# Optimization experiments

Hardware: AMD Instinct MI355X
Metric: run time of the kernel (lower is better)

Reference implementation:

```python
import jax, jax.numpy as jnp
import numpy as np

B, N, E = 4, 4096, 16384
D, A_DIM = 256, 64
T, HALF, STEPS, NTYPES = 16, 8, 3, 50


def setup_inputs() -> dict:
    key = jax.random.key(0)
    ks = jax.random.split(key, 16)
    s = 0.02  # small init so repeated DxD matmuls stay stable over 3 steps
    return {
        "annotation_id": jax.random.randint(ks[0], (B, N), 0, NTYPES),
        "src": jax.random.randint(ks[1], (B, E), 0, N),
        "dst": jax.random.randint(ks[2], (B, E), 0, N),
        "etype": jax.random.randint(ks[3], (B, E), 0, HALF),
        "edge_embed": jax.random.normal(ks[4], (T, D * D), jnp.float32) * s,
        "edge_bias": jax.random.normal(ks[5], (T, D), jnp.float32) * s,
        "type_embed": jax.random.normal(ks[6], (NTYPES, A_DIM), jnp.float32) * s,
        "Wr": jax.random.normal(ks[7], (D, 3 * D), jnp.float32) * s,
        "br": jnp.zeros((D,), jnp.float32),
        "Wz": jax.random.normal(ks[8], (D, 3 * D), jnp.float32) * s,
        "bz": jnp.zeros((D,), jnp.float32),
        "Wh": jax.random.normal(ks[9], (D, 3 * D), jnp.float32) * s,
        "bh": jnp.zeros((D,), jnp.float32),
        "Wa": jax.random.normal(ks[10], (1, D + A_DIM), jnp.float32) * s,
        "ba": jnp.zeros((1,), jnp.float32),
        "Wo": jax.random.normal(ks[11], (1, D + A_DIM), jnp.float32) * s,
        "bo": jnp.zeros((1,), jnp.float32),
    }


def reference(annotation_id, src, dst, etype, edge_embed, edge_bias, type_embed,
              Wr, br, Wz, bz, Wh, bh, Wa, ba, Wo, bo):
    # annotation: typeEmbed[id-1] if id>0 else zeros  -> [B, N, A_DIM]
    ann = jnp.where((annotation_id > 0)[..., None],
                    type_embed[jnp.clip(annotation_id - 1, 0, NTYPES - 1)],
                    jnp.zeros((), type_embed.dtype))
    # prop_state: annotation zero-padded to state_dim  -> [B, N, D]
    h = jnp.concatenate([ann, jnp.zeros((B, N, D - A_DIM), ann.dtype)], axis=-1)
    W = edge_embed.reshape(T, D, D)  # per-edge-type DxD matrices

    def step(h):
        # type-major projection: apply every edge-type matrix to every node state
        # P[b, t, n, :] = W[t] @ h[b, n]   -> [B, T, N, D]
        P = jnp.einsum('tij,bnj->btni', W, h)

        def per_graph(Pg, s_, d_, e_):
            # a_out[j]        += W[e] @ h[neighbour] + b[e]
            # a_in[neighbour] += W[e+HALF] @ h[j]   + b[e+HALF]
            m_out = Pg[e_, d_] + edge_bias[e_]            # [E, D]
            m_in = Pg[e_ + HALF, s_] + edge_bias[e_ + HALF]
            a_out = jnp.zeros((N, D), h.dtype).at[s_].add(m_out)
            a_in = jnp.zeros((N, D), h.dtype).at[d_].add(m_in)
            return a_in, a_out

        a_in, a_out = jax.vmap(per_graph)(P, src, dst, etype)
        # GRU-style propagator (dropout_rate = 0 -> identity)
        a = jnp.concatenate([a_in, a_out, h], axis=-1)    # [B, N, 3D]
        r = jax.nn.sigmoid(a @ Wr.T + br)
        z = jax.nn.sigmoid(a @ Wz.T + bz)
        h_hat = jnp.tanh(jnp.concatenate([a_in, a_out, r * h], axis=-1) @ Wh.T + bh)
        return (1.0 - z) * h + z * h_hat

    for _ in range(STEPS):
        h = step(h)

    join = jnp.concatenate([h, ann], axis=-1)             # [B, N, D+A]
    atten = jax.nn.sigmoid(join @ Wa.T + ba)              # [B, N, 1]
    ou = jnp.tanh(join @ Wo.T + bo)                       # [B, N, 1]
    w_sum = jnp.sum((atten * ou).reshape(-1, N), axis=1)  # [B]
    return jax.nn.sigmoid(w_sum)
```

## Files before the change

kernel.cpp:

```cpp
#include <hip/hip_runtime.h>
#include <cstdint>

#define BB 4
#define NN 4096
#define EE 16384
#define DD 256
#define ADIM 64
#define TT 16
#define HALFE 8
#define STEPS 3
#define OSTRIDE 4160
#define MAXTILES 1088
#define MAXM (MAXTILES * 128)

#define AS1 __attribute__((address_space(1)))
#define AS3 __attribute__((address_space(3)))

typedef __attribute__((ext_vector_type(8))) short short8;
typedef __attribute__((ext_vector_type(4))) float f32x4;

__device__ __forceinline__ float sigmoidf_(float x) { return 1.0f / (1.0f + __expf(-x)); }

__device__ __forceinline__ unsigned short f2bf(float x) {
    unsigned u = __float_as_uint(x);
    u += 0x7fffu + ((u >> 16) & 1u);
    return (unsigned short)(u >> 16);
}
__device__ __forceinline__ float bf2f(unsigned short b) {
    return __uint_as_float(((unsigned)b) << 16);
}

__global__ void prep_kernel(const int* __restrict__ ann_id, const float* __restrict__ type_embed,
                            const float* __restrict__ edge_embed, const float* __restrict__ Wr,
                            const float* __restrict__ Wz, const float* __restrict__ Wh,
                            float* __restrict__ ann, float* __restrict__ h,
                            unsigned short* __restrict__ hbf, unsigned short* __restrict__ Xbf,
                            unsigned short* __restrict__ W2bf, unsigned short* __restrict__ Wcatbf,
                            unsigned short* __restrict__ Whhbf, float* __restrict__ acc) {
    int bid = blockIdx.x, tid = threadIdx.x;
    if (bid < 4096) {
        if (bid == 0 && tid < 16) acc[tid] = 0.f;
        int idx = bid * 256 + tid;
        int bn = idx >> 6, q = idx & 63;
        int id = ann_id[bn];
        float4 v = {0.f, 0.f, 0.f, 0.f};
        if (q < 16) {
            if (id > 0) v = ((const float4*)(type_embed + (size_t)(id - 1) * ADIM))[q];
            ((float4*)(ann + (size_t)bn * ADIM))[q] = v;
        }
        ((float4*)(h + (size_t)bn * DD))[q] = v;
        ushort4 o;
        o.x = f2bf(v.x); o.y = f2bf(v.y); o.z = f2bf(v.z); o.w = f2bf(v.w);
        ((ushort4*)(hbf + (size_t)bn * DD))[q] = o;
        ((ushort4*)(Xbf + (size_t)bn * 768 + 512))[q] = o;
    } else if (bid < 5120) {
        int idx = (bid - 4096) * 256 + tid;
        float4 v = ((const float4*)edge_embed)[idx];
        ushort4 o;
        o.x = f2bf(v.x); o.y = f2bf(v.y); o.z = f2bf(v.z); o.w = f2bf(v.w);
        ((ushort4*)W2bf)[idx] = o;
    } else if (bid < 7424) {
        int idx = (bid - 5120) * 256 + tid;
        int c = idx / 768, k = idx % 768;
        float v;
        if (c < 256)       v = Wr[c * 768 + k];
        else if (c < 512)  v = Wz[(c - 256) * 768 + k];
        else               v = (k < 512) ? Wh[(c - 512) * 768 + k] : 0.f;
        Wcatbf[idx] = f2bf(v);
    } else {
        int idx = (bid - 7424) * 256 + tid;
        int i = idx / 256, k = idx % 256;
        Whhbf[idx] = f2bf(Wh[i * 768 + 512 + k]);
    }
}

__global__ void count_all(const int* __restrict__ src, const int* __restrict__ dst,
                          const int* __restrict__ et, int* __restrict__ counts,
                          int* __restrict__ c32) {
    __shared__ int cnt[32];
    int tid = threadIdx.x;
    if (tid < 32) cnt[tid] = 0;
    __syncthreads();
    int idx = blockIdx.x * 256 + tid;
    int b = idx >> 14;
    atomicAdd(&counts[(b * 2 + 0) * NN + src[idx]], 1);
    atomicAdd(&counts[(b * 2 + 1) * NN + dst[idx]], 1);
    atomicAdd(&cnt[b * 8 + et[idx]], 1);
    __syncthreads();
    if (tid < 32) atomicAdd(&c32[tid], cnt[tid]);
}

__global__ __launch_bounds__(1024) void scan_kernel(const int* __restrict__ counts,
                                                    int* __restrict__ offs,
                                                    int* __restrict__ cursor) {
    __shared__ int lsum[1024];
    int t = threadIdx.x, seg = blockIdx.x;
    int4 v = ((const int4*)(counts + (size_t)seg * NN))[t];
    int s1 = v.x + v.y, s2 = s1 + v.z, s3 = s2 + v.w;
    lsum[t] = s3;
    __syncthreads();
    for (int off = 1; off < 1024; off <<= 1) {
        int tmp = (t >= off) ? lsum[t - off] : 0;
        __syncthreads();
        lsum[t] += tmp;
        __syncthreads();
    }
    int base = lsum[t] - s3;
    int* o = offs + (size_t)seg * OSTRIDE;
    o[4 * t] = base; o[4 * t + 1] = base + v.x; o[4 * t + 2] = base + s1; o[4 * t + 3] = base + s2;
    if (t == 1023) o[4096] = lsum[1023];
    int* c = cursor + (size_t)seg * NN;
    c[4 * t] = base; c[4 * t + 1] = base + v.x; c[4 * t + 2] = base + s1; c[4 * t + 3] = base + s2;
}

__global__ void scan2_kernel(const int* __restrict__ c32, int* __restrict__ type_cursor,
                             int* __restrict__ tile_type, int* __restrict__ idx2) {
    __shared__ int pad[64];
    int t = threadIdx.x;
    for (int k = t; k < MAXTILES; k += 64) tile_type[k] = -1;
    __syncthreads();
    int b = t >> 4, dir = (t >> 3) & 1, tt = t & 7;
    int cnt = c32[b * 8 + tt];
    int padded = ((cnt + 127) >> 7) << 7;
    pad[t] = padded;
    __syncthreads();
    int off = 0;
    for (int k = 0; k < t; ++k) off += pad[k];
    type_cursor[t] = off;
    int t16 = dir * 8 + tt;
    int tile0 = off >> 7;
    for (int k = 0; k < (padded >> 7); ++k) tile_type[tile0 + k] = t16;
    for (int r = off + cnt; r < off + padded; ++r) idx2[r] = 0;
}

__global__ void fill2_kernel(const int* __restrict__ src, const int* __restrict__ dst,
                             const int* __restrict__ et, int* __restrict__ type_cursor,
                             int* __restrict__ node_cursor, int* __restrict__ entries,
                             int* __restrict__ idx2) {
    __shared__ int cnt[64];
    __shared__ int bse[64];
    int tid = threadIdx.x;
    if (tid < 64) cnt[tid] = 0;
    __syncthreads();
    int idx = blockIdx.x * 256 + tid;
    int b = idx >> 14;
    int s = src[idx], d = dst[idx], t = et[idx];
    int bin0 = b * 16 + t;
    int bin1 = b * 16 + 8 + t;
    int r0 = atomicAdd(&cnt[bin0], 1);
    int r1 = atomicAdd(&cnt[bin1], 1);
    __syncthreads();
    if (tid < 64) bse[tid] = atomicAdd(&type_cursor[tid], cnt[tid]);
    __syncthreads();
    int p0 = bse[bin0] + r0;
    int p1 = bse[bin1] + r1;
    idx2[p0] = b * NN + d;
    idx2[p1] = b * NN + s;
    int q0 = atomicAdd(&node_cursor[(b * 2 + 0) * NN + s], 1);
    entries[(size_t)(b * 2 + 0) * EE + q0] = (p0 << 4) | t;
    int q1 = atomicAdd(&node_cursor[(b * 2 + 1) * NN + d], 1);
    entries[(size_t)(b * 2 + 1) * EE + q1] = (p1 << 4) | (t + 8);
}


#define COMP_128x64(cb)                                                                 \
    _Pragma("unroll")                                                                   \
    for (int kk = 0; kk < 2; ++kk) {                                                    \
        short8 af[4], bfv[2];                                                           \
        _Pragma("unroll")                                                               \
        for (int m = 0; m < 4; ++m) {                                                   \
            int R = wr * 64 + m * 16 + lr;                                              \
            af[m] = *(const short8*)((const char*)As + (cb) * 16384 + R * 128 + (((kk * 4 + hi) ^ rx) << 4)); \
        }                                                                               \
        _Pragma("unroll")                                                               \
        for (int n = 0; n < 2; ++n) {                                                   \
            int R = wc * 32 + n * 16 + lr;                                              \
            bfv[n] = *(const short8*)((const char*)Bs + (cb) * 8192 + R * 128 + (((kk * 4 + hi) ^ rx) << 4)); \
        }                                                                               \
        _Pragma("unroll")                                                               \
        for (int m = 0; m < 4; ++m)                                                     \
            _Pragma("unroll")                                                           \
            for (int n = 0; n < 2; ++n)                                                 \
                acc[m][n] = __builtin_amdgcn_mfma_f32_16x16x32_bf16(bfv[n], af[m], acc[m][n], 0, 0, 0); \
    }

#define PIPE_WAIT(NSTR)                                                                 \
    asm volatile("s_waitcnt vmcnt(" NSTR ")" ::: "memory");                             \
    __builtin_amdgcn_s_barrier();                                                       \
    __builtin_amdgcn_sched_barrier(0);

__global__ __launch_bounds__(256) void gemm_msgs(const unsigned short* __restrict__ A,
                                                 const unsigned short* __restrict__ W2,
                                                 const int* __restrict__ idx2,
                                                 const int* __restrict__ tile_type,
                                                 unsigned short* __restrict__ C) {
    __shared__ __align__(16) unsigned short As[2 * 128 * 64];
    __shared__ __align__(16) unsigned short Bs[2 * 64 * 64];
    const int bid = blockIdx.x;
    const int wg = (bid & 7) * (MAXTILES * 4 / 8) + (bid >> 3);
    const int by = wg >> 2, bx = wg & 3;
    const int t16 = tile_type[by];
    if (t16 < 0) return;
    const int r0 = by << 7, c0 = bx << 6;
    const int tid = threadIdx.x;
    const int wv = tid >> 6, lane = tid & 63;
    const int wr = wv >> 1, wc = wv & 1;
    const int lr = lane & 15, hi = lane >> 4, rx = lane & 7;
    const int srow = wv * 8 + (lane >> 3);
    const int scol = ((lane & 7) ^ (lane >> 3)) << 3;
    int ar[4];
#pragma unroll
    for (int i = 0; i < 4; ++i) ar[i] = idx2[r0 + srow + i * 32];
    const unsigned short* Bg = W2 + (size_t)t16 * (DD * DD) + (size_t)(c0 + srow) * DD + scol;
    f32x4 acc[4][2] = {};
#define MS_STG(buf, kof)                                                                \
    { _Pragma("unroll")                                                                 \
      for (int i = 0; i < 4; ++i)                                                       \
          __builtin_amdgcn_global_load_lds(                                             \
              (const AS1 void*)(A + (size_t)ar[i] * DD + scol + (kof)),                 \
              (AS3 void*)((char*)As + (buf) * 16384 + wv * 1024 + i * 4096), 16, 0, 0); \
      _Pragma("unroll")                                                                 \
      for (int i = 0; i < 2; ++i)                                                       \
          __builtin_amdgcn_global_load_lds(                                             \
              (const AS1 void*)(Bg + (size_t)(i * 32) * DD + (kof)),                    \
              (AS3 void*)((char*)Bs + (buf) * 8192 + wv * 1024 + i * 4096), 16, 0, 0); }
    MS_STG(0, 0)
    for (int it = 0; it < 3; ++it) {
        MS_STG((it + 1) & 1, (it + 1) * 64)
        PIPE_WAIT("6")
        COMP_128x64(it & 1)
        __builtin_amdgcn_s_barrier();
    }
    PIPE_WAIT("0")
    COMP_128x64(1)
    const int erow = r0 + wr * 64 + lr;
    const int ecol = c0 + wc * 32 + (hi << 2);
#pragma unroll
    for (int m = 0; m < 4; ++m)
#pragma unroll
        for (int n = 0; n < 2; ++n) {
            ushort4 o;
            o.x = f2bf(acc[m][n][0]); o.y = f2bf(acc[m][n][1]);
            o.z = f2bf(acc[m][n][2]); o.w = f2bf(acc[m][n][3]);
            *(ushort4*)&C[(size_t)(erow + m * 16) * DD + ecol + n * 16] = o;
        }
}

__global__ __launch_bounds__(256) void gemm_rzu(const unsigned short* __restrict__ A,
                                                const unsigned short* __restrict__ Bt,
                                                const float* __restrict__ br,
                                                const float* __restrict__ bz,
                                                const float* __restrict__ h,
                                                unsigned short* __restrict__ RH,
                                                unsigned short* __restrict__ Zb,
                                                unsigned short* __restrict__ Ub) {
    __shared__ __align__(16) unsigned short As[2 * 128 * 64];
    __shared__ __align__(16) unsigned short Bs[2 * 64 * 64];
    const int bid = blockIdx.x;
    const int wg = (bid & 7) * 192 + (bid >> 3);
    const int bx = wg % 12, by = wg / 12;
    const int r0 = by << 7, c0 = bx << 6;
    const int tid = threadIdx.x;
    const int wv = tid >> 6, lane = tid & 63;
    const int wr = wv >> 1, wc = wv & 1;
    const int lr = lane & 15, hi = lane >> 4, rx = lane & 7;
    const int srow = wv * 8 + (lane >> 3);
    const int scol = ((lane & 7) ^ (lane >> 3)) << 3;
    const unsigned short* Ag = A + (size_t)(r0 + srow) * 768 + scol;
    const unsigned short* Bg = Bt + (size_t)(c0 + srow) * 768 + scol;
    f32x4 acc[4][2] = {};
#define RZ_STG(buf, kof)                                                                \
    { _Pragma("unroll")                                                                 \
      for (int i = 0; i < 4; ++i)                                                       \
          __builtin_amdgcn_global_load_lds(                                             \
              (const AS1 void*)(Ag + (size_t)(i * 32) * 768 + (kof)),                   \
              (AS3 void*)((char*)As + (buf) * 16384 + wv * 1024 + i * 4096), 16, 0, 0); \
      _Pragma("unroll")                                                                 \
      for (int i = 0; i < 2; ++i)                                                       \
          __builtin_amdgcn_global_load_lds(                                             \
              (const AS1 void*)(Bg + (size_t)(i * 32) * 768 + (kof)),                   \
              (AS3 void*)((char*)Bs + (buf) * 8192 + wv * 1024 + i * 4096), 16, 0, 0); }
    RZ_STG(0, 0)
    for (int it = 0; it < 11; ++it) {
        RZ_STG((it + 1) & 1, (it + 1) * 64)
        PIPE_WAIT("6")
        COMP_128x64(it & 1)
        __builtin_amdgcn_s_barrier();
    }
    PIPE_WAIT("0")
    COMP_128x64(1)
    const int erow = r0 + wr * 64 + lr;
    const int ecol = c0 + wc * 32 + (hi << 2);
    const int region = c0 >> 8;
#pragma unroll
    for (int m = 0; m < 4; ++m)
#pragma unroll
        for (int n = 0; n < 2; ++n) {
            int gr = erow + m * 16;
            int gc = ecol + n * 16;
            f32x4 v = acc[m][n];
            if (region == 0) {
                float4 bb = *(const float4*)&br[gc];
                float4 hv = *(const float4*)&h[(size_t)gr * 256 + gc];
                ushort4 o;
                o.x = f2bf(sigmoidf_(v[0] + bb.x) * hv.x);
                o.y = f2bf(sigmoidf_(v[1] + bb.y) * hv.y);
                o.z = f2bf(sigmoidf_(v[2] + bb.z) * hv.z);
                o.w = f2bf(sigmoidf_(v[3] + bb.w) * hv.w);
                *(ushort4*)&RH[(size_t)gr * 256 + gc] = o;
            } else if (region == 1) {
                int c = gc - 256;
                float4 bb = *(const float4*)&bz[c];
                ushort4 o;
                o.x = f2bf(sigmoidf_(v[0] + bb.x));
                o.y = f2bf(sigmoidf_(v[1] + bb.y));
                o.z = f2bf(sigmoidf_(v[2] + bb.z));
                o.w = f2bf(sigmoidf_(v[3] + bb.w));
                *(ushort4*)&Zb[(size_t)gr * 256 + c] = o;
            } else {
                int c = gc - 512;
                ushort4 o;
                o.x = f2bf(v[0]); o.y = f2bf(v[1]); o.z = f2bf(v[2]); o.w = f2bf(v[3]);
                *(ushort4*)&Ub[(size_t)gr * 256 + c] = o;
            }
        }
}

__global__ __launch_bounds__(256) void gemm_hh(const unsigned short* __restrict__ A,
                                               const unsigned short* __restrict__ Bt,
                                               const unsigned short* __restrict__ Zb,
                                               const unsigned short* __restrict__ Ub,
                                               const float* __restrict__ bh,
                                               float* __restrict__ h,
                                               unsigned short* __restrict__ hbf,
                                               unsigned short* __restrict__ Xbf) {
    __shared__ __align__(16) unsigned short As[2 * 64 * 64];
    __shared__ __align__(16) unsigned short Bs[2 * 64 * 64];
    const int bid = blockIdx.x;
    const int wg = (bid & 7) * 128 + (bid >> 3);
    const int by = wg >> 2, bx = wg & 3;
    const int r0 = by << 6, c0 = bx << 6;
    const int tid = threadIdx.x;
    const int wv = tid >> 6, lane = tid & 63;
    const int wr = wv >> 1, wc = wv & 1;
    const int lr = lane & 15, hi = lane >> 4, rx = lane & 7;
    const int srow = wv * 8 + (lane >> 3);
    const int scol = ((lane & 7) ^ (lane >> 3)) << 3;
    const unsigned short* Ag = A + (size_t)(r0 + srow) * 256 + scol;
    const unsigned short* Bg = Bt + (size_t)(c0 + srow) * 256 + scol;
    f32x4 acc[2][2] = {};
#define HH_STG(buf, kof)                                                                \
    { _Pragma("unroll")                                                                 \
      for (int i = 0; i < 2; ++i) {                                                     \
          __builtin_amdgcn_global_load_lds(                                             \
              (const AS1 void*)(Ag + (size_t)(i * 32) * 256 + (kof)),                   \
              (AS3 void*)((char*)As + (buf) * 8192 + wv * 1024 + i * 4096), 16, 0, 0);  \
          __builtin_amdgcn_global_load_lds(                                             \
              (const AS1 void*)(Bg + (size_t)(i * 32) * 256 + (kof)),                   \
              (AS3 void*)((char*)Bs + (buf) * 8192 + wv * 1024 + i * 4096), 16, 0, 0); } }
#define COMP_64x64(cb)                                                                  \
    _Pragma("unroll")                                                                   \
    for (int kk = 0; kk < 2; ++kk) {                                                    \
        short8 af[2], bfv[2];                                                           \
        _Pragma("unroll")                                                               \
        for (int m = 0; m < 2; ++m) {                                                   \
            int R = wr * 32 + m * 16 + lr;                                              \
            af[m] = *(const short8*)((const char*)As + (cb) * 8192 + R * 128 + (((kk * 4 + hi) ^ rx) << 4)); \
        }                                                                               \
        _Pragma("unroll")                                                               \
        for (int n = 0; n < 2; ++n) {                                                   \
            int R = wc * 32 + n * 16 + lr;                                              \
            bfv[n] = *(const short8*)((const char*)Bs + (cb) * 8192 + R * 128 + (((kk * 4 + hi) ^ rx) << 4)); \
        }                                                                               \
        _Pragma("unroll")                                                               \
        for (int m = 0; m < 2; ++m)                                                     \
            _Pragma("unroll")                                                           \
            for (int n = 0; n < 2; ++n)                                                 \
                acc[m][n] = __builtin_amdgcn_mfma_f32_16x16x32_bf16(bfv[n], af[m], acc[m][n], 0, 0, 0); \
    }
    HH_STG(0, 0)
    for (int it = 0; it < 3; ++it) {
        HH_STG((it + 1) & 1, (it + 1) * 64)
        PIPE_WAIT("4")
        COMP_64x64(it & 1)
        __builtin_amdgcn_s_barrier();
    }
    PIPE_WAIT("0")
    COMP_64x64(1)
    const int erow = r0 + wr * 32 + lr;
    const int ecol = c0 + wc * 32 + (hi << 2);
#pragma unroll
    for (int m = 0; m < 2; ++m)
#pragma unroll
        for (int n = 0; n < 2; ++n) {
            int gr = erow + m * 16;
            int gc = ecol + n * 16;
            size_t base = (size_t)gr * 256 + gc;
            f32x4 v = acc[m][n];
            float4 bb = *(const float4*)&bh[gc];
            float4 hv = *(const float4*)&h[base];
            ushort4 zp = *(const ushort4*)&Zb[base];
            ushort4 up = *(const ushort4*)&Ub[base];
            float4 hn;
            {
                float z = bf2f(zp.x); hn.x = (1.f - z) * hv.x + z * tanhf(bf2f(up.x) + v[0] + bb.x);
            }{
                float z = bf2f(zp.y); hn.y = (1.f - z) * hv.y + z * tanhf(bf2f(up.y) + v[1] + bb.y);
            }{
                float z = bf2f(zp.z); hn.z = (1.f - z) * hv.z + z * tanhf(bf2f(up.z) + v[2] + bb.z);
            }{
                float z = bf2f(zp.w); hn.w = (1.f - z) * hv.w + z * tanhf(bf2f(up.w) + v[3] + bb.w);
            }
            *(float4*)&h[base] = hn;
            ushort4 o;
            o.x = f2bf(hn.x); o.y = f2bf(hn.y); o.z = f2bf(hn.z); o.w = f2bf(hn.w);
            *(ushort4*)&hbf[base] = o;
            *(ushort4*)&Xbf[(size_t)gr * 768 + 512 + gc] = o;
        }
}

__global__ void gather2_kernel(const unsigned short* __restrict__ msgs,
                               const int* __restrict__ offs, const int* __restrict__ entries,
                               const float* __restrict__ bias, unsigned short* __restrict__ Xb) {
    int wv = threadIdx.x >> 6, lane = threadIdx.x & 63;
    int slot = blockIdx.x * 4 + wv;
    int b = slot >> 13;
    int dir = (slot >> 12) & 1;
    int node = slot & 4095;
    const int* o = offs + (size_t)(b * 2 + dir) * OSTRIDE;
    int beg = o[node], end = o[node + 1];
    const int* ent = entries + (size_t)(b * 2 + dir) * EE;
    const float4* bias4 = (const float4*)bias;
    float4 acc = {0.f, 0.f, 0.f, 0.f};
    for (int p = beg; p < end; ++p) {
        int e2 = ent[p];
        int row = e2 >> 4, t = e2 & 15;
        ushort4 pv = *(const ushort4*)(msgs + (size_t)row * DD + lane * 4);
        float4 bv = bias4[t * 64 + lane];
        acc.x += bf2f(pv.x) + bv.x;
        acc.y += bf2f(pv.y) + bv.y;
        acc.z += bf2f(pv.z) + bv.z;
        acc.w += bf2f(pv.w) + bv.w;
    }
    ushort4 o4;
    o4.x = f2bf(acc.x); o4.y = f2bf(acc.y); o4.z = f2bf(acc.z); o4.w = f2bf(acc.w);
    int colbase = (dir == 0 ? 256 : 0) + lane * 4;
    *(ushort4*)(Xb + ((size_t)b * NN + node) * 768 + colbase) = o4;
}

__global__ void final_reduce(const float* __restrict__ h, const float* __restrict__ ann,
                             const float* __restrict__ Wa, const float* __restrict__ ba,
                             const float* __restrict__ Wo, const float* __restrict__ bo,
                             float* __restrict__ acc) {
    int wv = threadIdx.x >> 6, lane = threadIdx.x & 63;
    int b = blockIdx.x >> 5;
    int nbase = (blockIdx.x & 31) * 128 + wv * 32;
    float4 wah = ((const float4*)Wa)[lane];
    float4 woh = ((const float4*)Wo)[lane];
    float4 waa = {0, 0, 0, 0}, woa = {0, 0, 0, 0};
    if (lane < 16) {
        waa = ((const float4*)(Wa + 256))[lane];
        woa = ((const float4*)(Wo + 256))[lane];
    }
    float bav = ba[0], bov = bo[0];
    float part = 0.f;
    for (int it = 0; it < 32; ++it) {
        int node = nbase + it;
        float4 hv = ((const float4*)(h + ((size_t)b * NN + node) * DD))[lane];
        float sa = hv.x * wah.x + hv.y * wah.y + hv.z * wah.z + hv.w * wah.w;
        float so = hv.x * woh.x + hv.y * woh.y + hv.z * woh.z + hv.w * woh.w;
        if (lane < 16) {
            float4 av = ((const float4*)(ann + ((size_t)b * NN + node) * ADIM))[lane];
            sa += av.x * waa.x + av.y * waa.y + av.z * waa.z + av.w * waa.w;
            so += av.x * woa.x + av.y * woa.y + av.z * woa.z + av.w * woa.w;
        }
        for (int off = 32; off; off >>= 1) {
            sa += __shfl_down(sa, off);
            so += __shfl_down(so, off);
        }
        if (lane == 0) part += sigmoidf_(sa + bav) * tanhf(so + bov);
    }
    if (lane == 0) atomicAdd(&acc[b], part);
}

__global__ void final_out(const float* __restrict__ acc, float* __restrict__ out) {
    int b = threadIdx.x;
    if (b < BB) out[b] = sigmoidf_(acc[b]);
}

extern "C" void kernel_launch(void* const* d_in, const int* in_sizes, int n_in,
                              void* d_out, int out_size, void* d_ws, size_t ws_size,
                              hipStream_t stream) {
    const int*   ann_id     = (const int*)d_in[0];
    const int*   src        = (const int*)d_in[1];
    const int*   dst        = (const int*)d_in[2];
    const int*   etype      = (const int*)d_in[3];
    const float* edge_embed = (const float*)d_in[4];
    const float* edge_bias  = (const float*)d_in[5];
    const float* type_embed = (const float*)d_in[6];
    const float* Wr = (const float*)d_in[7];
    const float* br = (const float*)d_in[8];
    const float* Wz = (const float*)d_in[9];
    const float* bz = (const float*)d_in[10];
    const float* Wh = (const float*)d_in[11];
    const float* bh = (const float*)d_in[12];
    const float* Wa = (const float*)d_in[13];
    const float* ba = (const float*)d_in[14];
    const float* Wo = (const float*)d_in[15];
    const float* bo = (const float*)d_in[16];
    float* out = (float*)d_out;

    char* base = (char*)d_ws;
    size_t off = 0;
    auto alloc = [&](size_t bytes) { char* p = base + off; off += (bytes + 255) & ~(size_t)255; return p; };
    float* ann  = (float*)alloc((size_t)BB * NN * ADIM * 4);
    float* h    = (float*)alloc((size_t)BB * NN * DD * 4);
    float* acc  = (float*)alloc(64);
    unsigned short* h_bf   = (unsigned short*)alloc((size_t)BB * NN * DD * 2);
    unsigned short* W2bf   = (unsigned short*)alloc((size_t)TT * DD * DD * 2);
    unsigned short* Wcatbf = (unsigned short*)alloc(768 * 768 * 2);
    unsigned short* Whhbf  = (unsigned short*)alloc(256 * 256 * 2);
    unsigned short* msgs   = (unsigned short*)alloc((size_t)MAXM * DD * 2);
    unsigned short* Xbf    = (unsigned short*)alloc((size_t)BB * NN * 768 * 2);
    unsigned short* RHbf   = (unsigned short*)alloc((size_t)BB * NN * DD * 2);
    unsigned short* Zb     = (unsigned short*)alloc((size_t)BB * NN * DD * 2);
    unsigned short* Ub     = (unsigned short*)alloc((size_t)BB * NN * DD * 2);
    int* counts  = (int*)alloc((size_t)BB * 2 * NN * 4);
    int* c32     = (int*)alloc(32 * 4);
    int* cursor  = (int*)alloc((size_t)BB * 2 * NN * 4);
    int* offsets = (int*)alloc((size_t)BB * 2 * OSTRIDE * 4);
    int* entries = (int*)alloc((size_t)BB * 2 * EE * 4);
    int* tcur    = (int*)alloc(64 * 4);
    int* ttype   = (int*)alloc(MAXTILES * 4);
    int* idx2    = (int*)alloc((size_t)MAXM * 4);

    prep_kernel<<<dim3(7680), dim3(256), 0, stream>>>(
        ann_id, type_embed, edge_embed, Wr, Wz, Wh,
        ann, h, h_bf, Xbf, W2bf, Wcatbf, Whhbf, acc);
    hipMemsetAsync(counts, 0, (size_t)BB * 2 * NN * 4 + 256, stream);
    count_all<<<dim3((BB * EE) / 256), dim3(256), 0, stream>>>(src, dst, etype, counts, c32);
    scan_kernel<<<dim3(BB * 2), dim3(1024), 0, stream>>>(counts, offsets, cursor);
    scan2_kernel<<<dim3(1), dim3(64), 0, stream>>>(c32, tcur, ttype, idx2);
    fill2_kernel<<<dim3((BB * EE) / 256), dim3(256), 0, stream>>>(
        src, dst, etype, tcur, cursor, entries, idx2);

    for (int s = 0; s < STEPS; ++s) {
        gemm_msgs<<<dim3(MAXTILES * 4), dim3(256), 0, stream>>>(
            h_bf, W2bf, idx2, ttype, msgs);
        gather2_kernel<<<dim3(BB * 2 * NN / 4), dim3(256), 0, stream>>>(
            msgs, offsets, entries, edge_bias, Xbf);
        gemm_rzu<<<dim3(1536), dim3(256), 0, stream>>>(
            Xbf, Wcatbf, br, bz, h, RHbf, Zb, Ub);
        gemm_hh<<<dim3(1024), dim3(256), 0, stream>>>(
            RHbf, Whhbf, Zb, Ub, bh, h, h_bf, Xbf);
    }

    final_reduce<<<dim3(128), dim3(256), 0, stream>>>(h, ann, Wa, ba, Wo, bo, acc);
    final_out<<<dim3(1), dim3(64), 0, stream>>>(acc, out);
}
```

Baseline: 410.8 us.

## Enlarge message and gate GEMM tiles to 256x64 with 512-thread blocks

The gathered-message GEMM and the r/z/u gate GEMM move from 128x64 tiles with 4 waves to 256x64 tiles with 8 waves. Per-type padding goes from 128 to 256 rows and the tile count and launch grids shrink to match. Each W tile loaded into LDS is now reused across twice as many rows, which cuts B-operand traffic and the number of blocks. The cost is more LDS per block, more padding waste per edge type, and fewer blocks to spread across CUs. The counts memset is also folded into the prep kernel to drop one launch.

```diff
diff --git a/kernel.cpp b/kernel.cpp
--- a/kernel.cpp
+++ b/kernel.cpp
@@ -10,8 +10,8 @@
 #define HALFE 8
 #define STEPS 3
 #define OSTRIDE 4160
-#define MAXTILES 1088
-#define MAXM (MAXTILES * 128)
+#define MT2 640
+#define MAXM (MT2 * 256)
 
 #define AS1 __attribute__((address_space(1)))
 #define AS3 __attribute__((address_space(3)))
@@ -36,9 +36,12 @@
                             float* __restrict__ ann, float* __restrict__ h,
                             unsigned short* __restrict__ hbf, unsigned short* __restrict__ Xbf,
                             unsigned short* __restrict__ W2bf, unsigned short* __restrict__ Wcatbf,
-                            unsigned short* __restrict__ Whhbf, float* __restrict__ acc) {
+                            unsigned short* __restrict__ Whhbf, float* __restrict__ acc,
+                            int* __restrict__ counts, int* __restrict__ c32) {
     int bid = blockIdx.x, tid = threadIdx.x;
     if (bid < 4096) {
+        if (bid < 128) counts[bid * 256 + tid] = 0;
+        if (bid == 0 && tid < 32) c32[tid] = 0;
         if (bid == 0 && tid < 16) acc[tid] = 0.f;
         int idx = bid * 256 + tid;
         int bn = idx >> 6, q = idx & 63;
@@ -117,19 +120,19 @@
                              int* __restrict__ tile_type, int* __restrict__ idx2) {
     __shared__ int pad[64];
     int t = threadIdx.x;
-    for (int k = t; k < MAXTILES; k += 64) tile_type[k] = -1;
+    for (int k = t; k < MT2; k += 64) tile_type[k] = -1;
     __syncthreads();
     int b = t >> 4, dir = (t >> 3) & 1, tt = t & 7;
     int cnt = c32[b * 8 + tt];
-    int padded = ((cnt + 127) >> 7) << 7;
+    int padded = ((cnt + 255) >> 8) << 8;
     pad[t] = padded;
     __syncthreads();
     int off = 0;
     for (int k = 0; k < t; ++k) off += pad[k];
     type_cursor[t] = off;
     int t16 = dir * 8 + tt;
-    int tile0 = off >> 7;
-    for (int k = 0; k < (padded >> 7); ++k) tile_type[tile0 + k] = t16;
+    int tile0 = off >> 8;
+    for (int k = 0; k < (padded >> 8); ++k) tile_type[tile0 + k] = t16;
     for (int r = off + cnt; r < off + padded; ++r) idx2[r] = 0;
 }
 
@@ -163,18 +166,23 @@
 }
 
 
-#define COMP_128x64(cb)                                                                 \
+#define PIPE_WAIT(NSTR)                                                                 \
+    asm volatile("s_waitcnt vmcnt(" NSTR ")" ::: "memory");                             \
+    __builtin_amdgcn_s_barrier();                                                       \
+    __builtin_amdgcn_sched_barrier(0);
+
+#define COMP_256x64(cb)                                                                 \
     _Pragma("unroll")                                                                   \
     for (int kk = 0; kk < 2; ++kk) {                                                    \
         short8 af[4], bfv[2];                                                           \
         _Pragma("unroll")                                                               \
         for (int m = 0; m < 4; ++m) {                                                   \
-            int R = wr * 64 + m * 16 + lr;                                              \
-            af[m] = *(const short8*)((const char*)As + (cb) * 16384 + R * 128 + (((kk * 4 + hi) ^ rx) << 4)); \
+            int R = wr4 * 64 + m * 16 + lr;                                             \
+            af[m] = *(const short8*)((const char*)As + (cb) * 32768 + R * 128 + (((kk * 4 + hi) ^ rx) << 4)); \
         }                                                                               \
         _Pragma("unroll")                                                               \
         for (int n = 0; n < 2; ++n) {                                                   \
-            int R = wc * 32 + n * 16 + lr;                                              \
+            int R = wc2 * 32 + n * 16 + lr;                                             \
             bfv[n] = *(const short8*)((const char*)Bs + (cb) * 8192 + R * 128 + (((kk * 4 + hi) ^ rx) << 4)); \
         }                                                                               \
         _Pragma("unroll")                                                               \
@@ -184,57 +192,50 @@
                 acc[m][n] = __builtin_amdgcn_mfma_f32_16x16x32_bf16(bfv[n], af[m], acc[m][n], 0, 0, 0); \
     }
 
-#define PIPE_WAIT(NSTR)                                                                 \
-    asm volatile("s_waitcnt vmcnt(" NSTR ")" ::: "memory");                             \
-    __builtin_amdgcn_s_barrier();                                                       \
-    __builtin_amdgcn_sched_barrier(0);
-
-__global__ __launch_bounds__(256) void gemm_msgs(const unsigned short* __restrict__ A,
+__global__ __launch_bounds__(512) void gemm_msgs(const unsigned short* __restrict__ A,
                                                  const unsigned short* __restrict__ W2,
                                                  const int* __restrict__ idx2,
                                                  const int* __restrict__ tile_type,
                                                  unsigned short* __restrict__ C) {
-    __shared__ __align__(16) unsigned short As[2 * 128 * 64];
+    __shared__ __align__(16) unsigned short As[2 * 256 * 64];
     __shared__ __align__(16) unsigned short Bs[2 * 64 * 64];
     const int bid = blockIdx.x;
-    const int wg = (bid & 7) * (MAXTILES * 4 / 8) + (bid >> 3);
+    const int wg = (bid & 7) * (MT2 * 4 / 8) + (bid >> 3);
     const int by = wg >> 2, bx = wg & 3;
     const int t16 = tile_type[by];
     if (t16 < 0) return;
-    const int r0 = by << 7, c0 = bx << 6;
+    const int r0 = by << 8, c0 = bx << 6;
     const int tid = threadIdx.x;
     const int wv = tid >> 6, lane = tid & 63;
-    const int wr = wv >> 1, wc = wv & 1;
+    const int wr4 = wv >> 1, wc2 = wv & 1;
     const int lr = lane & 15, hi = lane >> 4, rx = lane & 7;
-    const int srow = wv * 8 + (lane >> 3);
-    const int scol = ((lane & 7) ^ (lane >> 3)) << 3;
+    const int strow = tid >> 3;
+    const int scol = ((tid & 7) ^ ((tid >> 3) & 7)) << 3;
     int ar[4];
 #pragma unroll
-    for (int i = 0; i < 4; ++i) ar[i] = idx2[r0 + srow + i * 32];
-    const unsigned short* Bg = W2 + (size_t)t16 * (DD * DD) + (size_t)(c0 + srow) * DD + scol;
+    for (int i = 0; i < 4; ++i) ar[i] = idx2[r0 + i * 64 + strow];
+    const unsigned short* Bg = W2 + (size_t)t16 * (DD * DD) + (size_t)(c0 + strow) * DD + scol;
     f32x4 acc[4][2] = {};
 #define MS_STG(buf, kof)                                                                \
     { _Pragma("unroll")                                                                 \
       for (int i = 0; i < 4; ++i)                                                       \
           __builtin_amdgcn_global_load_lds(                                             \
               (const AS1 void*)(A + (size_t)ar[i] * DD + scol + (kof)),                 \
-              (AS3 void*)((char*)As + (buf) * 16384 + wv * 1024 + i * 4096), 16, 0, 0); \
-      _Pragma("unroll")                                                                 \
-      for (int i = 0; i < 2; ++i)                                                       \
-          __builtin_amdgcn_global_load_lds(                                             \
-              (const AS1 void*)(Bg + (size_t)(i * 32) * DD + (kof)),                    \
-              (AS3 void*)((char*)Bs + (buf) * 8192 + wv * 1024 + i * 4096), 16, 0, 0); }
+              (AS3 void*)((char*)As + (buf) * 32768 + i * 8192 + wv * 1024), 16, 0, 0); \
+      __builtin_amdgcn_global_load_lds(                                                 \
+          (const AS1 void*)(Bg + (kof)),                                                \
+          (AS3 void*)((char*)Bs + (buf) * 8192 + wv * 1024), 16, 0, 0); }
     MS_STG(0, 0)
     for (int it = 0; it < 3; ++it) {
         MS_STG((it + 1) & 1, (it + 1) * 64)
-        PIPE_WAIT("6")
-        COMP_128x64(it & 1)
+        PIPE_WAIT("5")
+        COMP_256x64(it & 1)
         __builtin_amdgcn_s_barrier();
     }
     PIPE_WAIT("0")
-    COMP_128x64(1)
-    const int erow = r0 + wr * 64 + lr;
-    const int ecol = c0 + wc * 32 + (hi << 2);
+    COMP_256x64(1)
+    const int erow = r0 + wr4 * 64 + lr;
+    const int ecol = c0 + wc2 * 32 + (hi << 2);
 #pragma unroll
     for (int m = 0; m < 4; ++m)
 #pragma unroll
@@ -246,7 +247,7 @@
         }
 }
 
-__global__ __launch_bounds__(256) void gemm_rzu(const unsigned short* __restrict__ A,
+__global__ __launch_bounds__(512) void gemm_rzu(const unsigned short* __restrict__ A,
                                                 const unsigned short* __restrict__ Bt,
                                                 const float* __restrict__ br,
                                                 const float* __restrict__ bz,
@@ -254,43 +255,41 @@
                                                 unsigned short* __restrict__ RH,
                                                 unsigned short* __restrict__ Zb,
                                                 unsigned short* __restrict__ Ub) {
-    __shared__ __align__(16) unsigned short As[2 * 128 * 64];
+    __shared__ __align__(16) unsigned short As[2 * 256 * 64];
     __shared__ __align__(16) unsigned short Bs[2 * 64 * 64];
     const int bid = blockIdx.x;
-    const int wg = (bid & 7) * 192 + (bid >> 3);
+    const int wg = (bid & 7) * 96 + (bid >> 3);
     const int bx = wg % 12, by = wg / 12;
-    const int r0 = by << 7, c0 = bx << 6;
+    const int r0 = by << 8, c0 = bx << 6;
     const int tid = threadIdx.x;
     const int wv = tid >> 6, lane = tid & 63;
-    const int wr = wv >> 1, wc = wv & 1;
+    const int wr4 = wv >> 1, wc2 = wv & 1;
     const int lr = lane & 15, hi = lane >> 4, rx = lane & 7;
-    const int srow = wv * 8 + (lane >> 3);
-    const int scol = ((lane & 7) ^ (lane >> 3)) << 3;
-    const unsigned short* Ag = A + (size_t)(r0 + srow) * 768 + scol;
-    const unsigned short* Bg = Bt + (size_t)(c0 + srow) * 768 + scol;
+    const int strow = tid >> 3;
+    const int scol = ((tid & 7) ^ ((tid >> 3) & 7)) << 3;
+    const unsigned short* Ag = A + (size_t)(r0 + strow) * 768 + scol;
+    const unsigned short* Bg = Bt + (size_t)(c0 + strow) * 768 + scol;
     f32x4 acc[4][2] = {};
 #define RZ_STG(buf, kof)                                                                \
     { _Pragma("unroll")                                                                 \
       for (int i = 0; i < 4; ++i)                                                       \
           __builtin_amdgcn_global_load_lds(                                             \
-              (const AS1 void*)(Ag + (size_t)(i * 32) * 768 + (kof)),                   \
-              (AS3 void*)((char*)As + (buf) * 16384 + wv * 1024 + i * 4096), 16, 0, 0); \
-      _Pragma("unroll")                                                                 \
-      for (int i = 0; i < 2; ++i)                                                       \
-          __builtin_amdgcn_global_load_lds(                                             \
-              (const AS1 void*)(Bg + (size_t)(i * 32) * 768 + (kof)),                   \
-              (AS3 void*)((char*)Bs + (buf) * 8192 + wv * 1024 + i * 4096), 16, 0, 0); }
+              (const AS1 void*)(Ag + (size_t)(i * 64) * 768 + (kof)),                   \
+              (AS3 void*)((char*)As + (buf) * 32768 + i * 8192 + wv * 1024), 16, 0, 0); \
+      __builtin_amdgcn_global_load_lds(                                                 \
+          (const AS1 void*)(Bg + (kof)),                                                \
+          (AS3 void*)((char*)Bs + (buf) * 8192 + wv * 1024), 16, 0, 0); }
     RZ_STG(0, 0)
     for (int it = 0; it < 11; ++it) {
         RZ_STG((it + 1) & 1, (it + 1) * 64)
-        PIPE_WAIT("6")
-        COMP_128x64(it & 1)
+        PIPE_WAIT("5")
+        COMP_256x64(it & 1)
         __builtin_amdgcn_s_barrier();
     }
     PIPE_WAIT("0")
-    COMP_128x64(1)
-    const int erow = r0 + wr * 64 + lr;
-    const int ecol = c0 + wc * 32 + (hi << 2);
+    COMP_256x64(1)
+    const int erow = r0 + wr4 * 64 + lr;
+    const int ecol = c0 + wc2 * 32 + (hi << 2);
     const int region = c0 >> 8;
 #pragma unroll
     for (int m = 0; m < 4; ++m)
@@ -339,7 +338,7 @@
     const int bid = blockIdx.x;
     const int wg = (bid & 7) * 128 + (bid >> 3);
     const int by = wg >> 2, bx = wg & 3;
-    const int r0 = by << 6, c0 = bx << 6;
+    const int r0 = wg >> 2 << 6, c0 = (wg & 3) << 6;
     const int tid = threadIdx.x;
     const int wv = tid >> 6, lane = tid & 63;
     const int wr = wv >> 1, wc = wv & 1;
@@ -531,13 +530,12 @@
     int* offsets = (int*)alloc((size_t)BB * 2 * OSTRIDE * 4);
     int* entries = (int*)alloc((size_t)BB * 2 * EE * 4);
     int* tcur    = (int*)alloc(64 * 4);
-    int* ttype   = (int*)alloc(MAXTILES * 4);
+    int* ttype   = (int*)alloc(MT2 * 4);
     int* idx2    = (int*)alloc((size_t)MAXM * 4);
 
     prep_kernel<<<dim3(7680), dim3(256), 0, stream>>>(
         ann_id, type_embed, edge_embed, Wr, Wz, Wh,
-        ann, h, h_bf, Xbf, W2bf, Wcatbf, Whhbf, acc);
-    hipMemsetAsync(counts, 0, (size_t)BB * 2 * NN * 4 + 256, stream);
+        ann, h, h_bf, Xbf, W2bf, Wcatbf, Whhbf, acc, counts, c32);
     count_all<<<dim3((BB * EE) / 256), dim3(256), 0, stream>>>(src, dst, etype, counts, c32);
     scan_kernel<<<dim3(BB * 2), dim3(1024), 0, stream>>>(counts, offsets, cursor);
     scan2_kernel<<<dim3(1), dim3(64), 0, stream>>>(c32, tcur, ttype, idx2);
@@ -545,11 +543,11 @@
         src, dst, etype, tcur, cursor, entries, idx2);
 
     for (int s = 0; s < STEPS; ++s) {
-        gemm_msgs<<<dim3(MAXTILES * 4), dim3(256), 0, stream>>>(
+        gemm_msgs<<<dim3(MT2 * 4), dim3(512), 0, stream>>>(
             h_bf, W2bf, idx2, ttype, msgs);
         gather2_kernel<<<dim3(BB * 2 * NN / 4), dim3(256), 0, stream>>>(
             msgs, offsets, entries, edge_bias, Xbf);
-        gemm_rzu<<<dim3(1536), dim3(256), 0, stream>>>(
+        gemm_rzu<<<dim3(768), dim3(512), 0, stream>>>(
             Xbf, Wcatbf, br, bz, h, RHbf, Zb, Ub);
         gemm_hh<<<dim3(1024), dim3(256), 0, stream>>>(
             RHbf, Whhbf, Zb, Ub, bh, h, h_bf, Xbf);
```

Result: slower. 421.9 us (+2.7%).

## Deduplicate per-type message rows via node/type claim map before message GEMM

Applied to the files above, without the earlier changes.

Adds a claim map keyed by (graph, edge type, node), so edges sharing the same type and endpoint share one message row instead of each getting their own. This shrinks the row count of the per-type message GEMM by removing duplicate W[t]·h[node] products, at the cost of atomic CAS claims in a 1 MB map that must be cleared every call. Map, count and type-counter resets move into the prep kernel, which replaces the separate memset. The GEMM global-to-LDS staging for the B operand is also re-indexed from per-thread row ids.

```diff
diff --git a/kernel.cpp b/kernel.cpp
--- a/kernel.cpp
+++ b/kernel.cpp
@@ -36,9 +36,14 @@
                             float* __restrict__ ann, float* __restrict__ h,
                             unsigned short* __restrict__ hbf, unsigned short* __restrict__ Xbf,
                             unsigned short* __restrict__ W2bf, unsigned short* __restrict__ Wcatbf,
-                            unsigned short* __restrict__ Whhbf, float* __restrict__ acc) {
+                            unsigned short* __restrict__ Whhbf, float* __restrict__ acc,
+                            int* __restrict__ counts, int* __restrict__ c32,
+                            int* __restrict__ map) {
     int bid = blockIdx.x, tid = threadIdx.x;
     if (bid < 4096) {
+        if (bid < 128) counts[bid * 256 + tid] = 0;
+        if (bid < 1024) map[bid * 256 + tid] = -1;
+        if (bid == 0 && tid < 64) c32[tid] = 0;
         if (bid == 0 && tid < 16) acc[tid] = 0.f;
         int idx = bid * 256 + tid;
         int bn = idx >> 6, q = idx & 63;
@@ -74,20 +79,24 @@
     }
 }
 
-__global__ void count_all(const int* __restrict__ src, const int* __restrict__ dst,
-                          const int* __restrict__ et, int* __restrict__ counts,
-                          int* __restrict__ c32) {
-    __shared__ int cnt[32];
-    int tid = threadIdx.x;
-    if (tid < 32) cnt[tid] = 0;
-    __syncthreads();
-    int idx = blockIdx.x * 256 + tid;
+__global__ void claim_kernel(const int* __restrict__ src, const int* __restrict__ dst,
+                             const int* __restrict__ et, int* __restrict__ counts,
+                             int* __restrict__ c32, int* __restrict__ map) {
+    int idx = blockIdx.x * 256 + threadIdx.x;
     int b = idx >> 14;
-    atomicAdd(&counts[(b * 2 + 0) * NN + src[idx]], 1);
-    atomicAdd(&counts[(b * 2 + 1) * NN + dst[idx]], 1);
-    atomicAdd(&cnt[b * 8 + et[idx]], 1);
-    __syncthreads();
-    if (tid < 32) atomicAdd(&c32[tid], cnt[tid]);
+    int s = src[idx], d = dst[idx], t = et[idx];
+    atomicAdd(&counts[(b * 2 + 0) * NN + s], 1);
+    atomicAdd(&counts[(b * 2 + 1) * NN + d], 1);
+    int k0 = (b << 16) | (t << 12) | d;
+    int k1 = (b << 16) | ((t + 8) << 12) | s;
+    if (atomicCAS(&map[k0], -1, -2) == -1) {
+        int r = atomicAdd(&c32[b * 16 + t], 1);
+        map[k0] = r;
+    }
+    if (atomicCAS(&map[k1], -1, -2) == -1) {
+        int r = atomicAdd(&c32[b * 16 + t + 8], 1);
+        map[k1] = r;
+    }
 }
 
 __global__ __launch_bounds__(1024) void scan_kernel(const int* __restrict__ counts,
@@ -119,41 +128,30 @@
     int t = threadIdx.x;
     for (int k = t; k < MAXTILES; k += 64) tile_type[k] = -1;
     __syncthreads();
-    int b = t >> 4, dir = (t >> 3) & 1, tt = t & 7;
-    int cnt = c32[b * 8 + tt];
+    int cnt = c32[t];
     int padded = ((cnt + 127) >> 7) << 7;
     pad[t] = padded;
     __syncthreads();
     int off = 0;
     for (int k = 0; k < t; ++k) off += pad[k];
     type_cursor[t] = off;
-    int t16 = dir * 8 + tt;
+    int t16 = t & 15;
     int tile0 = off >> 7;
     for (int k = 0; k < (padded >> 7); ++k) tile_type[tile0 + k] = t16;
     for (int r = off + cnt; r < off + padded; ++r) idx2[r] = 0;
 }
 
-__global__ void fill2_kernel(const int* __restrict__ src, const int* __restrict__ dst,
-                             const int* __restrict__ et, int* __restrict__ type_cursor,
+__global__ void fill3_kernel(const int* __restrict__ src, const int* __restrict__ dst,
+                             const int* __restrict__ et, const int* __restrict__ type_cursor,
                              int* __restrict__ node_cursor, int* __restrict__ entries,
-                             int* __restrict__ idx2) {
-    __shared__ int cnt[64];
-    __shared__ int bse[64];
-    int tid = threadIdx.x;
-    if (tid < 64) cnt[tid] = 0;
-    __syncthreads();
-    int idx = blockIdx.x * 256 + tid;
+                             int* __restrict__ idx2, const int* __restrict__ map) {
+    int idx = blockIdx.x * 256 + threadIdx.x;
     int b = idx >> 14;
     int s = src[idx], d = dst[idx], t = et[idx];
-    int bin0 = b * 16 + t;
-    int bin1 = b * 16 + 8 + t;
-    int r0 = atomicAdd(&cnt[bin0], 1);
-    int r1 = atomicAdd(&cnt[bin1], 1);
-    __syncthreads();
-    if (tid < 64) bse[tid] = atomicAdd(&type_cursor[tid], cnt[tid]);
-    __syncthreads();
-    int p0 = bse[bin0] + r0;
-    int p1 = bse[bin1] + r1;
+    int k0 = (b << 16) | (t << 12) | d;
+    int k1 = (b << 16) | ((t + 8) << 12) | s;
+    int p0 = type_cursor[b * 16 + t] + map[k0];
+    int p1 = type_cursor[b * 16 + t + 8] + map[k1];
     idx2[p0] = b * NN + d;
     idx2[p1] = b * NN + s;
     int q0 = atomicAdd(&node_cursor[(b * 2 + 0) * NN + s], 1);
@@ -161,7 +159,6 @@
     int q1 = atomicAdd(&node_cursor[(b * 2 + 1) * NN + d], 1);
     entries[(size_t)(b * 2 + 1) * EE + q1] = (p1 << 4) | (t + 8);
 }
-
 
 #define COMP_128x64(cb)                                                                 \
     _Pragma("unroll")                                                                   \
@@ -206,12 +203,12 @@
     const int wv = tid >> 6, lane = tid & 63;
     const int wr = wv >> 1, wc = wv & 1;
     const int lr = lane & 15, hi = lane >> 4, rx = lane & 7;
-    const int srow = wv * 8 + (lane >> 3);
-    const int scol = ((lane & 7) ^ (lane >> 3)) << 3;
+    const int strow = tid >> 3;
+    const int scol = ((tid & 7) ^ ((tid >> 3) & 7)) << 3;
     int ar[4];
 #pragma unroll
-    for (int i = 0; i < 4; ++i) ar[i] = idx2[r0 + srow + i * 32];
-    const unsigned short* Bg = W2 + (size_t)t16 * (DD * DD) + (size_t)(c0 + srow) * DD + scol;
+    for (int i = 0; i < 4; ++i) ar[i] = idx2[r0 + strow + i * 32];
+    const unsigned short* Bg = W2 + (size_t)t16 * (DD * DD) + (size_t)(c0 + strow) * DD + scol;
     f32x4 acc[4][2] = {};
 #define MS_STG(buf, kof)                                                                \
     { _Pragma("unroll")                                                                 \
@@ -219,11 +216,12 @@
           __builtin_amdgcn_global_load_lds(                                             \
               (const AS1 void*)(A + (size_t)ar[i] * DD + scol + (kof)),                 \
               (AS3 void*)((char*)As + (buf) * 16384 + wv * 1024 + i * 4096), 16, 0, 0); \
-      _Pragma("unroll")                                                                 \
-      for (int i = 0; i < 2; ++i)                                                       \
-          __builtin_amdgcn_global_load_lds(                                             \
-              (const AS1 void*)(Bg + (size_t)(i * 32) * DD + (kof)),                    \
-              (AS3 void*)((char*)Bs + (buf) * 8192 + wv * 1024 + i * 4096), 16, 0, 0); }
+      __builtin_amdgcn_global_load_lds(                                                 \
+          (const AS1 void*)(Bg + (kof)),                                                \
+          (AS3 void*)((char*)Bs + (buf) * 8192 + wv * 1024 + ((tid >> 8) & 1) * 4096), 16, 0, 0); \
+      __builtin_amdgcn_global_load_lds(                                                 \
+          (const AS1 void*)(Bg + (size_t)32 * DD + (kof)),                              \
+          (AS3 void*)((char*)Bs + (buf) * 8192 + wv * 1024 + 4096), 16, 0, 0); }
     MS_STG(0, 0)
     for (int it = 0; it < 3; ++it) {
         MS_STG((it + 1) & 1, (it + 1) * 64)
@@ -264,10 +262,10 @@
     const int wv = tid >> 6, lane = tid & 63;
     const int wr = wv >> 1, wc = wv & 1;
     const int lr = lane & 15, hi = lane >> 4, rx = lane & 7;
-    const int srow = wv * 8 + (lane >> 3);
-    const int scol = ((lane & 7) ^ (lane >> 3)) << 3;
-    const unsigned short* Ag = A + (size_t)(r0 + srow) * 768 + scol;
-    const unsigned short* Bg = Bt + (size_t)(c0 + srow) * 768 + scol;
+    const int strow = tid >> 3;
+    const int scol = ((tid & 7) ^ ((tid >> 3) & 7)) << 3;
+    const unsigned short* Ag = A + (size_t)(r0 + strow) * 768 + scol;
+    const unsigned short* Bg = Bt + (size_t)(c0 + strow) * 768 + scol;
     f32x4 acc[4][2] = {};
 #define RZ_STG(buf, kof)                                                                \
     { _Pragma("unroll")                                                                 \
@@ -275,11 +273,12 @@
           __builtin_amdgcn_global_load_lds(                                             \
               (const AS1 void*)(Ag + (size_t)(i * 32) * 768 + (kof)),                   \
               (AS3 void*)((char*)As + (buf) * 16384 + wv * 1024 + i * 4096), 16, 0, 0); \
-      _Pragma("unroll")                                                                 \
-      for (int i = 0; i < 2; ++i)                                                       \
-          __builtin_amdgcn_global_load_lds(                                             \
-              (const AS1 void*)(Bg + (size_t)(i * 32) * 768 + (kof)),                   \
-              (AS3 void*)((char*)Bs + (buf) * 8192 + wv * 1024 + i * 4096), 16, 0, 0); }
+      __builtin_amdgcn_global_load_lds(                                                 \
+          (const AS1 void*)(Bg + (kof)),                                                \
+          (AS3 void*)((char*)Bs + (buf) * 8192 + wv * 1024), 16, 0, 0);                 \
+      __builtin_amdgcn_global_load_lds(                                                 \
+          (const AS1 void*)(Bg + (size_t)32 * 768 + (kof)),                             \
+          (AS3 void*)((char*)Bs + (buf) * 8192 + wv * 1024 + 4096), 16, 0, 0); }
     RZ_STG(0, 0)
     for (int it = 0; it < 11; ++it) {
         RZ_STG((it + 1) & 1, (it + 1) * 64)
@@ -338,8 +337,7 @@
     __shared__ __align__(16) unsigned short Bs[2 * 64 * 64];
     const int bid = blockIdx.x;
     const int wg = (bid & 7) * 128 + (bid >> 3);
-    const int by = wg >> 2, bx = wg & 3;
-    const int r0 = by << 6, c0 = bx << 6;
+    const int r0 = wg >> 2 << 6, c0 = (wg & 3) << 6;
     const int tid = threadIdx.x;
     const int wv = tid >> 6, lane = tid & 63;
     const int wr = wv >> 1, wc = wv & 1;
@@ -526,23 +524,24 @@
     unsigned short* Zb     = (unsigned short*)alloc((size_t)BB * NN * DD * 2);
     unsigned short* Ub     = (unsigned short*)alloc((size_t)BB * NN * DD * 2);
     int* counts  = (int*)alloc((size_t)BB * 2 * NN * 4);
-    int* c32     = (int*)alloc(32 * 4);
+    int* c32     = (int*)alloc(64 * 4);
     int* cursor  = (int*)alloc((size_t)BB * 2 * NN * 4);
     int* offsets = (int*)alloc((size_t)BB * 2 * OSTRIDE * 4);
     int* entries = (int*)alloc((size_t)BB * 2 * EE * 4);
     int* tcur    = (int*)alloc(64 * 4);
     int* ttype   = (int*)alloc(MAXTILES * 4);
     int* idx2    = (int*)alloc((size_t)MAXM * 4);
+    int* map     = (int*)alloc((size_t)262144 * 4);
 
     prep_kernel<<<dim3(7680), dim3(256), 0, stream>>>(
         ann_id, type_embed, edge_embed, Wr, Wz, Wh,
-        ann, h, h_bf, Xbf, W2bf, Wcatbf, Whhbf, acc);
-    hipMemsetAsync(counts, 0, (size_t)BB * 2 * NN * 4 + 256, stream);
-    count_all<<<dim3((BB * EE) / 256), dim3(256), 0, stream>>>(src, dst, etype, counts, c32);
+        ann, h, h_bf, Xbf, W2bf, Wcatbf, Whhbf, acc, counts, c32, map);
+    claim_kernel<<<dim3((BB * EE) / 256), dim3(256), 0, stream>>>(
+        src, dst, etype, counts, c32, map);
     scan_kernel<<<dim3(BB * 2), dim3(1024), 0, stream>>>(counts, offsets, cursor);
     scan2_kernel<<<dim3(1), dim3(64), 0, stream>>>(c32, tcur, ttype, idx2);
-    fill2_kernel<<<dim3((BB * EE) / 256), dim3(256), 0, stream>>>(
-        src, dst, etype, tcur, cursor, entries, idx2);
+    fill3_kernel<<<dim3((BB * EE) / 256), dim3(256), 0, stream>>>(
+        src, dst, etype, tcur, cursor, entries, idx2, map);
 
     for (int s = 0; s < STEPS; ++s) {
         gemm_msgs<<<dim3(MAXTILES * 4), dim3(256), 0, stream>>>(
```

New measurement: 574.0 us. 1.4x slower.
